# Kernel optimization log

Hardware: AMD Instinct MI355X
Metric: run time of the kernel (lower is better)

## Reference

```python
import jax, jax.numpy as jnp
import numpy as np

D_MODEL = 512
NUM_HEADS = 8
HEAD_DIM = D_MODEL // NUM_HEADS
SEQ_LEN = 4096
BATCH = 2
D_FF = 4 * D_MODEL
EPS = 1e-5


def _layer_norm(x, g, b):
    mu = jnp.mean(x, axis=-1, keepdims=True)
    var = jnp.var(x, axis=-1, keepdims=True)
    return (x - mu) * jax.lax.rsqrt(var + EPS) * g + b


def setup_inputs() -> dict:
    key = jax.random.key(0)
    ks = jax.random.split(key, 12)
    s = 0.02
    inp = {
        "x": jax.random.normal(ks[0], (BATCH, SEQ_LEN, D_MODEL), jnp.float32),
        # Linear weights stored as [in, out] (y = x @ W + b)
        "Wq": jax.random.normal(ks[1], (D_MODEL, D_MODEL), jnp.float32) * s,
        "bq": jnp.zeros((D_MODEL,), jnp.float32),
        "Wk": jax.random.normal(ks[2], (D_MODEL, D_MODEL), jnp.float32) * s,
        "bk": jnp.zeros((D_MODEL,), jnp.float32),
        "Wv": jax.random.normal(ks[3], (D_MODEL, D_MODEL), jnp.float32) * s,
        "bv": jnp.zeros((D_MODEL,), jnp.float32),
        "Wo": jax.random.normal(ks[4], (D_MODEL, D_MODEL), jnp.float32) * s,
        "bo": jnp.zeros((D_MODEL,), jnp.float32),
        "ln1_g": jnp.ones((D_MODEL,), jnp.float32),
        "ln1_b": jnp.zeros((D_MODEL,), jnp.float32),
        "ln2_g": jnp.ones((D_MODEL,), jnp.float32),
        "ln2_b": jnp.zeros((D_MODEL,), jnp.float32),
        "W1": jax.random.normal(ks[5], (D_MODEL, D_FF), jnp.float32) * s,
        "b1": jnp.zeros((D_FF,), jnp.float32),
        "W2": jax.random.normal(ks[6], (D_FF, D_MODEL), jnp.float32) * s,
        "b2": jnp.zeros((D_MODEL,), jnp.float32),
    }
    return inp


def reference(x, Wq, bq, Wk, bk, Wv, bv, Wo, bo, ln1_g, ln1_b, ln2_g, ln2_b, W1, b1, W2, b2):
    B, S, D = x.shape
    residual = x
    h = _layer_norm(x, ln1_g, ln1_b)
    # project and split heads: [B, H, S, Dh]
    def split_heads(t):
        return t.reshape(B, S, NUM_HEADS, HEAD_DIM).transpose(0, 2, 1, 3)
    q = split_heads(h @ Wq + bq)
    k = split_heads(h @ Wk + bk)
    v = split_heads(h @ Wv + bv)
    scores = jnp.einsum("bhqd,bhkd->bhqk", q, k) / (HEAD_DIM ** 0.5)
    attn = jax.nn.softmax(scores, axis=-1)
    out = jnp.einsum("bhqk,bhkd->bhqd", attn, v)
    out = out.transpose(0, 2, 1, 3).reshape(B, S, D)
    out = out @ Wo + bo
    x1 = residual + out
    h2 = _layer_norm(x1, ln2_g, ln2_b)
    ff = jax.nn.gelu(h2 @ W1 + b1, approximate=False) @ W2 + b2
    return x1 + ff
```

## Files before the change

kernel.cpp:

```cpp
#include <hip/hip_runtime.h>
#include <hip/hip_bf16.h>
#include <math.h>

typedef __hip_bfloat16 bf16;

#define D_MODEL 512
#define NUM_HEADS 8
#define HEAD_DIM 64
#define SEQ_LEN 4096
#define BATCH 2
#define D_FF 2048
#define TOKENS (BATCH * SEQ_LEN)
#define QKV_STRIDE 1536
#define KSPLIT 2

typedef short short4v __attribute__((ext_vector_type(4)));
typedef short short8v __attribute__((ext_vector_type(8)));
typedef float float4v __attribute__((ext_vector_type(4)));

union frag_u { short8v v8; short4v v4[2]; short s[8]; };
union pack_u { unsigned u[2]; short4v v4; };

__device__ __forceinline__ float b2f(bf16 v) { return __bfloat162float(v); }
__device__ __forceinline__ bf16 f2b(float v) { return __float2bfloat16(v); }
__device__ __forceinline__ short f2bs(float v) { bf16 t = __float2bfloat16(v); return *(short*)&t; }
__device__ __forceinline__ float exp2fast(float x) { return __builtin_amdgcn_exp2f(x); }

__device__ __forceinline__ unsigned pack_bf16(float lo, float hi) {
    unsigned a = __float_as_uint(hi) + 0x8000u;
    unsigned b = __float_as_uint(lo) + 0x8000u;
    return __builtin_amdgcn_perm(a, b, 0x07060302u);
}

#define AS1(p) ((__attribute__((address_space(1))) void*)(p))
#define AS3(p) ((__attribute__((address_space(3))) void*)(p))

__device__ __forceinline__ int self_detect(const unsigned* __restrict__ xw, int tid) {
    unsigned w = xw[tid & 63];
    unsigned e = (w >> 7) & 0xFFu;
    unsigned long long b = __ballot(e >= 110 && e <= 140);
    return __popcll(b) < 32;
}

__device__ __forceinline__ void do_tr(const void* __restrict__ src, bf16* __restrict__ dst,
                                      int K, int N, int n0, int k0, int fl, int tid,
                                      bf16 (*tile)[65]) {
    int c = tid & 63, r4 = tid >> 6;
#pragma unroll
    for (int t = 0; t < 16; t++) {
        int r = t * 4 + r4;
        size_t si = (size_t)(k0 + r) * N + n0 + c;
        float v = fl ? ((const float*)src)[si] : b2f(((const bf16*)src)[si]);
        tile[r][c] = f2b(v);
    }
    __syncthreads();
#pragma unroll
    for (int t = 0; t < 16; t++) {
        int r = t * 4 + r4;
        dst[(size_t)(n0 + r) * K + k0 + c] = tile[c][r];
    }
}

__global__ void prep_kernel(const void* x, const void* Wq, const void* Wk, const void* Wv,
                            const void* Wo, const void* W1, const void* W2,
                            const void* bq, const void* bk, const void* bv, const void* bo,
                            const void* b1, const void* b2,
                            const void* g1, const void* e1, const void* g2, const void* e2,
                            bf16* __restrict__ Wqkvt ,
                            bf16* __restrict__ W1t, bf16* __restrict__ W2t,
                            bf16* __restrict__ small, int* __restrict__ flag) {
    __shared__ bf16 tile[64][65];
    int blk = blockIdx.x, tid = threadIdx.x;
    int fl = self_detect((const unsigned*)x, tid);
    if (blk == 0 && tid == 0) flag[0] = fl;
    if (blk < 256) {
        int z = blk >> 6, tt = blk & 63;
        const void* src = (z == 0) ? Wq : (z == 1) ? Wk : (z == 2) ? Wv : Wo;
        do_tr(src, Wqkvt + (size_t)z * 512 * 512, 512, 512, (tt & 7) * 64, (tt >> 3) * 64,
              fl, tid, tile);
    } else if (blk < 512) {
        int tt = blk - 256;
        do_tr(W1, W1t, 512, 2048, (tt & 31) * 64, (tt >> 5) * 64, fl, tid, tile);
    } else if (blk < 768) {
        int tt = blk - 512;
        do_tr(W2, W2t, 2048, 512, (tt & 7) * 64, (tt >> 3) * 64, fl, tid, tile);
    } else {
        int i = (blk - 768) * 256 + tid;
        const void* src; int off;
        if (i < 512)       { src = bq; off = 0; }
        else if (i < 1024) { src = bk; off = 512; }
        else if (i < 1536) { src = bv; off = 1024; }
        else if (i < 2048) { src = bo; off = 1536; }
        else if (i < 4096) { src = b1; off = 2048; }
        else if (i < 4608) { src = b2; off = 4096; }
        else if (i < 5120) { src = g1; off = 4608; }
        else if (i < 5632) { src = e1; off = 5120; }
        else if (i < 6144) { src = g2; off = 5632; }
        else               { src = e2; off = 6144; }
        int j = i - off;
        small[i] = fl ? f2b(((const float*)src)[j]) : ((const bf16*)src)[j];
    }
}

template <int MODE>
__global__ void ln_kernel(const void* __restrict__ xv, const bf16* __restrict__ g,
                          const bf16* __restrict__ b, bf16* __restrict__ out,
                          const int* __restrict__ flag) {
    int t = blockIdx.x;
    int tid = threadIdx.x;
    int fl = (MODE == 2) ? *flag : 0;
    float v0, v1;
    if (fl) {
        const float* xr = (const float*)xv + (size_t)t * D_MODEL;
        v0 = xr[tid]; v1 = xr[tid + 256];
    } else {
        const bf16* xr = (const bf16*)xv + (size_t)t * D_MODEL;
        v0 = b2f(xr[tid]); v1 = b2f(xr[tid + 256]);
    }
    float s = v0 + v1, ss = v0 * v0 + v1 * v1;
    for (int o = 32; o > 0; o >>= 1) {
        s += __shfl_down(s, o);
        ss += __shfl_down(ss, o);
    }
    __shared__ float rs[4], rss[4], stat[2];
    int w = tid >> 6, l = tid & 63;
    if (l == 0) { rs[w] = s; rss[w] = ss; }
    __syncthreads();
    if (tid == 0) {
        float S = rs[0] + rs[1] + rs[2] + rs[3];
        float SS = rss[0] + rss[1] + rss[2] + rss[3];
        float mu = S / (float)D_MODEL;
        float var = SS / (float)D_MODEL - mu * mu;
        stat[0] = mu;
        stat[1] = rsqrtf(var + 1e-5f);
    }
    __syncthreads();
    float mu = stat[0], rstd = stat[1];
    bf16* orow = out + (size_t)t * D_MODEL;
    orow[tid]       = f2b((v0 - mu) * rstd * b2f(g[tid])       + b2f(b[tid]));
    orow[tid + 256] = f2b((v1 - mu) * rstd * b2f(g[tid + 256]) + b2f(b[tid + 256]));
}

__device__ __forceinline__ float gelu_tanh(float v) {
    float u = 0.7978845608f * (v + 0.044715f * v * v * v);
    float e2 = __expf(-2.f * u);
    return v / (1.f + e2);
}

template <int ACT>
__global__ __launch_bounds__(256) void mfma_gemm(
    const bf16* __restrict__ A, const bf16* __restrict__ Wt,
    const bf16* __restrict__ bias, bf16* __restrict__ Cout,
    int M, int N, int K) {
    __shared__ bf16 As[128 * 64];
    __shared__ bf16 Bs[128 * 64];
    int tid = threadIdx.x, wave = tid >> 6, lane = tid & 63;
    int m = lane & 15, g = lane >> 4;
    int row0 = blockIdx.y * 128, col0 = blockIdx.x * 128;
    int R0 = (wave >> 1) * 64, C0 = (wave & 1) * 64;
    float4v acc[4][4] = {};

    int srow = lane >> 3;
    int scol = (lane & 7) * 8;
    const bf16* Ab = A  + (size_t)(row0 + wave * 8 + srow) * K + scol;
    const bf16* Bb = Wt + (size_t)(col0 + wave * 8 + srow) * K + scol;

    for (int k0 = 0; k0 < K; k0 += 64) {
#pragma unroll
        for (int t = 0; t < 4; t++) {
            int rbase = t * 32 + wave * 8;
            __builtin_amdgcn_global_load_lds(AS1(Ab + (size_t)(t * 32) * K + k0),
                                             AS3(&As[rbase * 64]), 16, 0, 0);
            __builtin_amdgcn_global_load_lds(AS1(Bb + (size_t)(t * 32) * K + k0),
                                             AS3(&Bs[rbase * 64]), 16, 0, 0);
        }
        __syncthreads();
#pragma unroll
        for (int kk = 0; kk < 2; kk++) {
            short8v fa[4], fb[4];
#pragma unroll
            for (int i = 0; i < 4; i++)
                fa[i] = *(const short8v*)&As[(R0 + i * 16 + m) * 64 + kk * 32 + g * 8];
#pragma unroll
            for (int j = 0; j < 4; j++)
                fb[j] = *(const short8v*)&Bs[(C0 + j * 16 + m) * 64 + kk * 32 + g * 8];
#pragma unroll
            for (int i = 0; i < 4; i++)
#pragma unroll
                for (int j = 0; j < 4; j++)
                    acc[i][j] = __builtin_amdgcn_mfma_f32_16x16x32_bf16(fa[i], fb[j], acc[i][j], 0, 0, 0);
        }
        __syncthreads();
    }

#pragma unroll
    for (int i = 0; i < 4; i++) {
#pragma unroll
        for (int r = 0; r < 4; r++) {
            int row = row0 + R0 + i * 16 + g * 4 + r;
#pragma unroll
            for (int j = 0; j < 4; j++) {
                int col = col0 + C0 + j * 16 + m;
                float v = acc[i][j][r] + b2f(bias[col]);
                if (ACT == 1) v = gelu_tanh(v);
                Cout[(size_t)row * N + col] = f2b(v);
            }
        }
    }
}

template <int RES, int OUTMODE>
__global__ __launch_bounds__(256) void mfma_gemm64(
    const bf16* __restrict__ A, const bf16* __restrict__ Wt,
    const bf16* __restrict__ bias, const void* __restrict__ res,
    void* __restrict__ Cout, const int* __restrict__ flag, int M, int N, int K) {
    __shared__ bf16 As[128 * 64];
    __shared__ bf16 Bs[64 * 64];
    int tid = threadIdx.x, wave = tid >> 6, lane = tid & 63;
    int m = lane & 15, g = lane >> 4;
    int row0 = blockIdx.y * 128, col0 = blockIdx.x * 64;
    int R0 = wave * 32;
    int fl = (OUTMODE == 2 || RES == 3) ? *flag : 0;
    float4v acc[2][4] = {};

    int srow = lane >> 3;
    int scol = (lane & 7) * 8;
    const bf16* Ab = A  + (size_t)(row0 + wave * 8 + srow) * K + scol;
    const bf16* Bb = Wt + (size_t)(col0 + wave * 8 + srow) * K + scol;

    for (int k0 = 0; k0 < K; k0 += 64) {
#pragma unroll
        for (int t = 0; t < 4; t++) {
            __builtin_amdgcn_global_load_lds(AS1(Ab + (size_t)(t * 32) * K + k0),
                                             AS3(&As[(t * 32 + wave * 8) * 64]), 16, 0, 0);
            if (t < 2)
                __builtin_amdgcn_global_load_lds(AS1(Bb + (size_t)(t * 32) * K + k0),
                                                 AS3(&Bs[(t * 32 + wave * 8) * 64]), 16, 0, 0);
        }
        __syncthreads();
#pragma unroll
        for (int kk = 0; kk < 2; kk++) {
            short8v fa[2], fb[4];
#pragma unroll
            for (int i = 0; i < 2; i++)
                fa[i] = *(const short8v*)&As[(R0 + i * 16 + m) * 64 + kk * 32 + g * 8];
#pragma unroll
            for (int j = 0; j < 4; j++)
                fb[j] = *(const short8v*)&Bs[(j * 16 + m) * 64 + kk * 32 + g * 8];
#pragma unroll
            for (int i = 0; i < 2; i++)
#pragma unroll
                for (int j = 0; j < 4; j++)
                    acc[i][j] = __builtin_amdgcn_mfma_f32_16x16x32_bf16(fa[i], fb[j], acc[i][j], 0, 0, 0);
        }
        __syncthreads();
    }

#pragma unroll
    for (int i = 0; i < 2; i++) {
#pragma unroll
        for (int r = 0; r < 4; r++) {
            int row = row0 + R0 + i * 16 + g * 4 + r;
#pragma unroll
            for (int j = 0; j < 4; j++) {
                int col = col0 + j * 16 + m;
                float v = acc[i][j][r] + b2f(bias[col]);
                size_t idx = (size_t)row * N + col;
                if (RES == 2) v += b2f(((const bf16*)res)[idx]);
                if (RES == 3) v += fl ? ((const float*)res)[idx]
                                      : b2f(((const bf16*)res)[idx]);
                if (OUTMODE == 0) ((bf16*)Cout)[idx] = f2b(v);
                else {
                    if (fl) ((float*)Cout)[idx] = v;
                    else ((bf16*)Cout)[idx] = f2b(v);
                }
            }
        }
    }
}

__global__ void v_transpose(const bf16* __restrict__ qkv, bf16* __restrict__ Vt_g) {
    __shared__ bf16 tile[64][65];
    int s0 = blockIdx.x * 64;
    int bh = blockIdx.y;
    int b = bh >> 3, h = bh & 7;
    int c = threadIdx.x & 63, r4 = threadIdx.x >> 6;
    const bf16* src = qkv + ((size_t)b * SEQ_LEN + s0) * QKV_STRIDE + 1024 + h * 64;
#pragma unroll
    for (int t = 0; t < 16; t++) {
        int r = t * 4 + r4;
        tile[r][c] = src[(size_t)r * QKV_STRIDE + c];
    }
    __syncthreads();
    bf16* dst = Vt_g + (size_t)bh * 64 * SEQ_LEN + s0;
#pragma unroll
    for (int t = 0; t < 16; t++) {
        int r = t * 4 + r4;
        dst[(size_t)r * SEQ_LEN + c] = tile[c][r];
    }
}

__global__ __launch_bounds__(256, 4) void flash_attn(const bf16* __restrict__ Q,
                                                     const bf16* __restrict__ K,
                                                     const bf16* __restrict__ Vt_g,
                                                     bf16* __restrict__ Op,
                                                     float2* __restrict__ mlout) {
    __shared__ bf16 Ks[64][72];
    __shared__ bf16 Vt[64][68];
    __shared__ bf16 Pt[4][32][72];

    int tid = threadIdx.x;
    int wave = tid >> 6, lane = tid & 63;
    int m = lane & 15, g = lane >> 4;

    int bh = blockIdx.y;
    size_t base = (size_t)(bh >> 3) * SEQ_LEN * QKV_STRIDE + (size_t)(bh & 7) * HEAD_DIM;
    int q0w = blockIdx.x * 128 + wave * 32;

    const float qscale = 0.125f * 1.44269504f;
    short8v aQ[2][2];
#pragma unroll
    for (int mt = 0; mt < 2; mt++) {
        const bf16* qp = Q + base + (size_t)(q0w + mt * 16 + m) * QKV_STRIDE + g * 8;
#pragma unroll
        for (int c = 0; c < 2; c++) {
            frag_u u;
#pragma unroll
            for (int j = 0; j < 8; j++) u.s[j] = f2bs(b2f(qp[c * 32 + j]) * qscale);
            aQ[mt][c] = u.v8;
        }
    }

    float mrow[2] = {-1e30f, -1e30f};
    float lrow[2] = {0.f, 0.f};
    float4v oacc[2][4] = {};

    int sk = tid >> 2, sd = (tid & 3) * 16;
    int vrow = tid >> 2, vcol = (tid & 3) * 16;

    const unsigned short* Ku = (const unsigned short*)(K + base);
    const unsigned short* Vg = (const unsigned short*)Vt_g +
                               (size_t)bh * 64 * SEQ_LEN + (size_t)vrow * SEQ_LEN;

    int t0 = blockIdx.z * (64 / KSPLIT);
    int t1 = t0 + 64 / KSPLIT;
    for (int t = t0; t < t1; t++) {
        int kt0 = t * 64;
        __syncthreads();
        {
            const unsigned short* kp = Ku + (size_t)(kt0 + sk) * QKV_STRIDE + sd;
            *(short8v*)&Ks[sk][sd]     = *(const short8v*)(kp);
            *(short8v*)&Ks[sk][sd + 8] = *(const short8v*)(kp + 8);
        }
        {
            frag_u u0, u1;
            u0.v8 = *(const short8v*)(Vg + kt0 + vcol);
            u1.v8 = *(const short8v*)(Vg + kt0 + vcol + 8);
            *(short4v*)&Vt[vrow][vcol]      = u0.v4[0];
            *(short4v*)&Vt[vrow][vcol + 4]  = u0.v4[1];
            *(short4v*)&Vt[vrow][vcol + 8]  = u1.v4[0];
            *(short4v*)&Vt[vrow][vcol + 12] = u1.v4[1];
        }
        __syncthreads();

        float4v st[2][4];
#pragma unroll
        for (int kt = 0; kt < 4; kt++) {
            short8v bK0 = *(const short8v*)&Ks[kt * 16 + m][g * 8];
            short8v bK1 = *(const short8v*)&Ks[kt * 16 + m][32 + g * 8];
#pragma unroll
            for (int mt = 0; mt < 2; mt++) {
                float4v a = {0.f, 0.f, 0.f, 0.f};
                a = __builtin_amdgcn_mfma_f32_16x16x32_bf16(bK0, aQ[mt][0], a, 0, 0, 0);
                a = __builtin_amdgcn_mfma_f32_16x16x32_bf16(bK1, aQ[mt][1], a, 0, 0, 0);
                st[mt][kt] = a;
            }
        }

#pragma unroll
        for (int mt = 0; mt < 2; mt++) {
            float tm = st[mt][0][0];
#pragma unroll
            for (int kt = 0; kt < 4; kt++)
#pragma unroll
                for (int r = 0; r < 4; r++) tm = fmaxf(tm, st[mt][kt][r]);
            tm = fmaxf(tm, __shfl_xor(tm, 16));
            tm = fmaxf(tm, __shfl_xor(tm, 32));
            float mnew = fmaxf(mrow[mt], tm);
            float alpha = exp2fast(mrow[mt] - mnew);
            mrow[mt] = mnew;

            float psum = 0.f;
#pragma unroll
            for (int kt = 0; kt < 4; kt++) {
                float p0 = exp2fast(st[mt][kt][0] - mnew);
                float p1 = exp2fast(st[mt][kt][1] - mnew);
                float p2 = exp2fast(st[mt][kt][2] - mnew);
                float p3 = exp2fast(st[mt][kt][3] - mnew);
                psum += (p0 + p1) + (p2 + p3);
                pack_u pp;
                pp.u[0] = pack_bf16(p0, p1);
                pp.u[1] = pack_bf16(p2, p3);
                *(short4v*)&Pt[wave][mt * 16 + m][kt * 16 + g * 4] = pp.v4;
            }
            lrow[mt] = lrow[mt] * alpha + psum;
#pragma unroll
            for (int dt = 0; dt < 4; dt++)
#pragma unroll
                for (int r = 0; r < 4; r++) oacc[mt][dt][r] *= alpha;
        }

        short8v bP[2][2];
#pragma unroll
        for (int mt = 0; mt < 2; mt++)
#pragma unroll
            for (int c = 0; c < 2; c++)
                bP[mt][c] = *(const short8v*)&Pt[wave][mt * 16 + m][c * 32 + g * 8];

#pragma unroll
        for (int dt = 0; dt < 4; dt++) {
#pragma unroll
            for (int c = 0; c < 2; c++) {
                frag_u u;
                u.v4[0] = *(const short4v*)&Vt[dt * 16 + m][c * 32 + g * 8];
                u.v4[1] = *(const short4v*)&Vt[dt * 16 + m][c * 32 + g * 8 + 4];
#pragma unroll
                for (int mt = 0; mt < 2; mt++)
                    oacc[mt][dt] = __builtin_amdgcn_mfma_f32_16x16x32_bf16(u.v8, bP[mt][c], oacc[mt][dt], 0, 0, 0);
            }
        }
    }

    size_t zoff = (size_t)blockIdx.z * NUM_HEADS * BATCH + bh;
    size_t pbase = zoff * (SEQ_LEN * (size_t)HEAD_DIM);
#pragma unroll
    for (int mt = 0; mt < 2; mt++) {
        float l = lrow[mt];
        l += __shfl_xor(l, 16);
        l += __shfl_xor(l, 32);
        int q = q0w + mt * 16 + m;
        bf16* orow = Op + pbase + (size_t)q * HEAD_DIM;
#pragma unroll
        for (int dt = 0; dt < 4; dt++) {
            pack_u oo;
            oo.u[0] = pack_bf16(oacc[mt][dt][0], oacc[mt][dt][1]);
            oo.u[1] = pack_bf16(oacc[mt][dt][2], oacc[mt][dt][3]);
            *(short4v*)&orow[dt * 16 + g * 4] = oo.v4;
        }
        if (g == 0) mlout[zoff * SEQ_LEN + q] = make_float2(mrow[mt], l);
    }
}

__global__ void attn_merge(const bf16* __restrict__ Op, const float2* __restrict__ ml,
                           bf16* __restrict__ O) {
    int i = blockIdx.x * 256 + threadIdx.x;
    int d = i & 63;
    int q = (i >> 6) & (SEQ_LEN - 1);
    int bh = i >> 18;
    const int HQ = NUM_HEADS * BATCH * SEQ_LEN;
    float2 a0 = ml[bh * SEQ_LEN + q];
    float2 a1 = ml[HQ + bh * SEQ_LEN + q];
    float M = fmaxf(a0.x, a1.x);
    float w0 = exp2fast(a0.x - M), w1 = exp2fast(a1.x - M);
    float inv = 1.f / (a0.y * w0 + a1.y * w1);
    const size_t NP = (size_t)HQ * HEAD_DIM;
    float o = (b2f(Op[i]) * w0 + b2f(Op[NP + i]) * w1) * inv;
    O[((size_t)((bh >> 3) * SEQ_LEN + q)) * D_MODEL + (bh & 7) * HEAD_DIM + d] = f2b(o);
}

extern "C" void kernel_launch(void* const* d_in, const int* in_sizes, int n_in,
                              void* d_out, int out_size, void* d_ws, size_t ws_size,
                              hipStream_t stream) {
    const void* x     = d_in[0];
    const void* Wq    = d_in[1];
    const void* bq    = d_in[2];
    const void* Wk    = d_in[3];
    const void* bk    = d_in[4];
    const void* Wv    = d_in[5];
    const void* bv    = d_in[6];
    const void* Wo    = d_in[7];
    const void* bo    = d_in[8];
    const void* ln1_g = d_in[9];
    const void* ln1_b = d_in[10];
    const void* ln2_g = d_in[11];
    const void* ln2_b = d_in[12];
    const void* W1    = d_in[13];
    const void* b1    = d_in[14];
    const void* W2    = d_in[15];
    const void* b2    = d_in[16];

    char* p = (char*)d_ws;
    int* flag = (int*)p;                      p += 256;
    size_t tok_d = (size_t)TOKENS * D_MODEL;
    char* region2 = p;                        p += 2 * tok_d * 2;
    bf16* x1b   = (bf16*)region2;
    bf16* hb    = (bf16*)(region2 + tok_d * 2);
    bf16* Opart = (bf16*)region2;
    bf16*  bigA = (bf16*)p;                   p += (size_t)TOKENS * D_FF * 2;
    bf16*  qkvb = bigA;
    bf16*  ab   = bigA + (size_t)TOKENS * QKV_STRIDE;
    bf16*  ffb  = bigA;
    bf16*  Wqkvt = (bf16*)p;                  p += (size_t)QKV_STRIDE * D_MODEL * 2;
    bf16*  Wot   = (bf16*)p;                  p += (size_t)D_MODEL * D_MODEL * 2;
    bf16*  W1t   = (bf16*)p;                  p += (size_t)D_FF * D_MODEL * 2;
    bf16*  W2t   = (bf16*)p;                  p += (size_t)D_MODEL * D_FF * 2;
    bf16*  Vtg   = (bf16*)p;                  p += (size_t)NUM_HEADS * BATCH * HEAD_DIM * SEQ_LEN * 2;
    float2* mlb  = (float2*)p;                p += (size_t)KSPLIT * NUM_HEADS * BATCH * SEQ_LEN * sizeof(float2);
    bf16*  small = (bf16*)p;                  p += 6656 * 2;
    bf16* bias_qkv = small + 0;
    bf16* bias_o   = small + 1536;
    bf16* b1b      = small + 2048;
    bf16* b2b      = small + 4096;
    bf16* g1b      = small + 4608;
    bf16* be1b     = small + 5120;
    bf16* g2b      = small + 5632;
    bf16* be2b     = small + 6144;

    prep_kernel<<<794, 256, 0, stream>>>(x, Wq, Wk, Wv, Wo, W1, W2,
                                         bq, bk, bv, bo, b1, b2,
                                         ln1_g, ln1_b, ln2_g, ln2_b,
                                         Wqkvt, W1t, W2t, small, flag);

    ln_kernel<2><<<TOKENS, 256, 0, stream>>>(x, g1b, be1b, hb, flag);

    mfma_gemm<0><<<dim3(QKV_STRIDE / 128, TOKENS / 128), 256, 0, stream>>>(
        hb, Wqkvt, bias_qkv, qkvb, TOKENS, QKV_STRIDE, D_MODEL);

    v_transpose<<<dim3(SEQ_LEN / 64, NUM_HEADS * BATCH), 256, 0, stream>>>(qkvb, Vtg);

    flash_attn<<<dim3(SEQ_LEN / 128, 16, KSPLIT), 256, 0, stream>>>(
        qkvb, qkvb + 512, Vtg, Opart, mlb);
    attn_merge<<<(NUM_HEADS * BATCH * SEQ_LEN * HEAD_DIM) / 256, 256, 0, stream>>>(
        Opart, mlb, ab);

    mfma_gemm64<3, 0><<<dim3(D_MODEL / 64, TOKENS / 128), 256, 0, stream>>>(
        ab, Wot, bias_o, x, x1b, flag, TOKENS, D_MODEL, D_MODEL);

    ln_kernel<0><<<TOKENS, 256, 0, stream>>>(x1b, g2b, be2b, hb, flag);

    mfma_gemm<1><<<dim3(D_FF / 128, TOKENS / 128), 256, 0, stream>>>(
        hb, W1t, b1b, ffb, TOKENS, D_FF, D_MODEL);

    mfma_gemm64<2, 2><<<dim3(D_MODEL / 64, TOKENS / 128), 256, 0, stream>>>(
        ffb, W2t, b2b, x1b, d_out, flag, TOKENS, D_MODEL, D_FF);
}
```

Baseline: 370.4 us.

## Prefetch next K/V tile into registers, add lazy softmax rescale and MFMA priority

The attention loop now loads the next K and V tile from global memory into registers before computing on the current tile, then writes them to shared memory after the PV MFMAs. This overlaps global latency with compute. The online softmax skips the rescale of the output accumulator and running sum unless the row max has grown by more than a threshold, which cuts exp and multiply work. s_setprio raises wave priority around the MFMA blocks. The trade-offs are extra registers, which may lower occupancy, and probabilities computed against a stale max that can reach 2^8.

New measurement: 369.1 us. Within noise of the previous version (-0.3%).

```diff
diff --git a/kernel.cpp b/kernel.cpp
--- a/kernel.cpp
+++ b/kernel.cpp
@@ -344,26 +344,37 @@
 
     int t0 = blockIdx.z * (64 / KSPLIT);
     int t1 = t0 + 64 / KSPLIT;
+
+    short8v rk0, rk1, rv0, rv1;
+    {
+        int kt0 = t0 * 64;
+        const unsigned short* kp = Ku + (size_t)(kt0 + sk) * QKV_STRIDE + sd;
+        rk0 = *(const short8v*)(kp);
+        rk1 = *(const short8v*)(kp + 8);
+        rv0 = *(const short8v*)(Vg + kt0 + vcol);
+        rv1 = *(const short8v*)(Vg + kt0 + vcol + 8);
+        *(short8v*)&Ks[sk][sd]     = rk0;
+        *(short8v*)&Ks[sk][sd + 8] = rk1;
+        frag_u u0, u1; u0.v8 = rv0; u1.v8 = rv1;
+        *(short4v*)&Vt[vrow][vcol]      = u0.v4[0];
+        *(short4v*)&Vt[vrow][vcol + 4]  = u0.v4[1];
+        *(short4v*)&Vt[vrow][vcol + 8]  = u1.v4[0];
+        *(short4v*)&Vt[vrow][vcol + 12] = u1.v4[1];
+    }
+    __syncthreads();
+
     for (int t = t0; t < t1; t++) {
-        int kt0 = t * 64;
-        __syncthreads();
-        {
-            const unsigned short* kp = Ku + (size_t)(kt0 + sk) * QKV_STRIDE + sd;
-            *(short8v*)&Ks[sk][sd]     = *(const short8v*)(kp);
-            *(short8v*)&Ks[sk][sd + 8] = *(const short8v*)(kp + 8);
-        }
-        {
-            frag_u u0, u1;
-            u0.v8 = *(const short8v*)(Vg + kt0 + vcol);
-            u1.v8 = *(const short8v*)(Vg + kt0 + vcol + 8);
-            *(short4v*)&Vt[vrow][vcol]      = u0.v4[0];
-            *(short4v*)&Vt[vrow][vcol + 4]  = u0.v4[1];
-            *(short4v*)&Vt[vrow][vcol + 8]  = u1.v4[0];
-            *(short4v*)&Vt[vrow][vcol + 12] = u1.v4[1];
-        }
-        __syncthreads();
+        if (t + 1 < t1) {
+            int ktn = (t + 1) * 64;
+            const unsigned short* kp = Ku + (size_t)(ktn + sk) * QKV_STRIDE + sd;
+            rk0 = *(const short8v*)(kp);
+            rk1 = *(const short8v*)(kp + 8);
+            rv0 = *(const short8v*)(Vg + ktn + vcol);
+            rv1 = *(const short8v*)(Vg + ktn + vcol + 8);
+        }
 
         float4v st[2][4];
+        __builtin_amdgcn_s_setprio(1);
 #pragma unroll
         for (int kt = 0; kt < 4; kt++) {
             short8v bK0 = *(const short8v*)&Ks[kt * 16 + m][g * 8];
@@ -376,38 +387,46 @@
                 st[mt][kt] = a;
             }
         }
+        __builtin_amdgcn_s_setprio(0);
 
 #pragma unroll
         for (int mt = 0; mt < 2; mt++) {
-            float tm = st[mt][0][0];
-#pragma unroll
-            for (int kt = 0; kt < 4; kt++)
-#pragma unroll
-                for (int r = 0; r < 4; r++) tm = fmaxf(tm, st[mt][kt][r]);
+            float a0 = fmaxf(fmaxf(st[mt][0][0], st[mt][0][1]),
+                             fmaxf(st[mt][0][2], st[mt][0][3]));
+            float a1 = fmaxf(fmaxf(st[mt][1][0], st[mt][1][1]),
+                             fmaxf(st[mt][1][2], st[mt][1][3]));
+            float a2 = fmaxf(fmaxf(st[mt][2][0], st[mt][2][1]),
+                             fmaxf(st[mt][2][2], st[mt][2][3]));
+            float a3 = fmaxf(fmaxf(st[mt][3][0], st[mt][3][1]),
+                             fmaxf(st[mt][3][2], st[mt][3][3]));
+            float tm = fmaxf(fmaxf(a0, a1), fmaxf(a2, a3));
             tm = fmaxf(tm, __shfl_xor(tm, 16));
             tm = fmaxf(tm, __shfl_xor(tm, 32));
-            float mnew = fmaxf(mrow[mt], tm);
-            float alpha = exp2fast(mrow[mt] - mnew);
-            mrow[mt] = mnew;
-
+            if (!__all(tm - mrow[mt] <= 8.f)) {
+                float mnew = fmaxf(mrow[mt], tm);
+                float alpha = exp2fast(mrow[mt] - mnew);
+                mrow[mt] = mnew;
+                lrow[mt] *= alpha;
+#pragma unroll
+                for (int dt = 0; dt < 4; dt++)
+#pragma unroll
+                    for (int r = 0; r < 4; r++) oacc[mt][dt][r] *= alpha;
+            }
+            float mcur = mrow[mt];
             float psum = 0.f;
 #pragma unroll
             for (int kt = 0; kt < 4; kt++) {
-                float p0 = exp2fast(st[mt][kt][0] - mnew);
-                float p1 = exp2fast(st[mt][kt][1] - mnew);
-                float p2 = exp2fast(st[mt][kt][2] - mnew);
-                float p3 = exp2fast(st[mt][kt][3] - mnew);
+                float p0 = exp2fast(st[mt][kt][0] - mcur);
+                float p1 = exp2fast(st[mt][kt][1] - mcur);
+                float p2 = exp2fast(st[mt][kt][2] - mcur);
+                float p3 = exp2fast(st[mt][kt][3] - mcur);
                 psum += (p0 + p1) + (p2 + p3);
                 pack_u pp;
                 pp.u[0] = pack_bf16(p0, p1);
                 pp.u[1] = pack_bf16(p2, p3);
                 *(short4v*)&Pt[wave][mt * 16 + m][kt * 16 + g * 4] = pp.v4;
             }
-            lrow[mt] = lrow[mt] * alpha + psum;
-#pragma unroll
-            for (int dt = 0; dt < 4; dt++)
-#pragma unroll
-                for (int r = 0; r < 4; r++) oacc[mt][dt][r] *= alpha;
+            lrow[mt] += psum;
         }
 
         short8v bP[2][2];
@@ -417,6 +436,7 @@
             for (int c = 0; c < 2; c++)
                 bP[mt][c] = *(const short8v*)&Pt[wave][mt * 16 + m][c * 32 + g * 8];
 
+        __builtin_amdgcn_s_setprio(1);
 #pragma unroll
         for (int dt = 0; dt < 4; dt++) {
 #pragma unroll
@@ -429,6 +449,19 @@
                     oacc[mt][dt] = __builtin_amdgcn_mfma_f32_16x16x32_bf16(u.v8, bP[mt][c], oacc[mt][dt], 0, 0, 0);
             }
         }
+        __builtin_amdgcn_s_setprio(0);
+
+        __syncthreads();
+        if (t + 1 < t1) {
+            *(short8v*)&Ks[sk][sd]     = rk0;
+            *(short8v*)&Ks[sk][sd + 8] = rk1;
+            frag_u u0, u1; u0.v8 = rv0; u1.v8 = rv1;
+            *(short4v*)&Vt[vrow][vcol]      = u0.v4[0];
+            *(short4v*)&Vt[vrow][vcol + 4]  = u0.v4[1];
+            *(short4v*)&Vt[vrow][vcol + 8]  = u1.v4[0];
+            *(short4v*)&Vt[vrow][vcol + 12] = u1.v4[1];
+        }
+        __syncthreads();
     }
 
     size_t zoff = (size_t)blockIdx.z * NUM_HEADS * BATCH + bh;
```
